# Optimization experiments

Measured on AMD Instinct MI355X. Metric: run time of the kernel, lower is better.

## Reference

```python
import jax, jax.numpy as jnp
import numpy as np

B, QLEN, DIM = 16, 1, 4096
H, HKV, HD = 32, 8, 128  # n_heads, n_kv_heads, head_dim
PREFIX = 8192            # tokens already in the static KV cache


def setup_inputs() -> dict:
    key = jax.random.key(0)
    ks = jax.random.split(key, 7)
    s = 0.02
    return {
        "x": jax.random.normal(ks[0], (B, QLEN, DIM), jnp.float32),
        "cache_k": jax.random.normal(ks[1], (B, PREFIX, HKV, HD), jnp.float32),
        "cache_v": jax.random.normal(ks[2], (B, PREFIX, HKV, HD), jnp.float32),
        "wq": jax.random.normal(ks[3], (H * HD, DIM), jnp.float32) * s,
        "wk": jax.random.normal(ks[4], (HKV * HD, DIM), jnp.float32) * s,
        "wv": jax.random.normal(ks[5], (HKV * HD, DIM), jnp.float32) * s,
        "wo": jax.random.normal(ks[6], (DIM, H * HD), jnp.float32) * s,
    }


def reference(x, cache_k, cache_v, wq, wk, wv, wo):
    """Decode step of AttentionWithKVCache (static cache, GQA).

    Equivalent to: write new K/V at start_pos=PREFIX, attend q over
    cache[:, :PREFIX+QLEN], repeat_kv to expand kv heads, SDPA, out proj.
    """
    b, s, _ = x.shape
    q = (x @ wq.T).reshape(b, s, H, HD)        # [B,S,H,D]
    k_new = (x @ wk.T).reshape(b, s, HKV, HD)  # [B,S,Hkv,D]
    v_new = (x @ wv.T).reshape(b, s, HKV, HD)
    # cache write == concat of prefix with new tokens
    k = jnp.concatenate([cache_k, k_new], axis=1)  # [B,K,Hkv,D]
    v = jnp.concatenate([cache_v, v_new], axis=1)
    rep = H // HKV
    # repeat_kv: expand+reshape repeats each kv head `rep` times consecutively
    k = jnp.repeat(k, rep, axis=2)  # [B,K,H,D]
    v = jnp.repeat(v, rep, axis=2)
    scale = 1.0 / jnp.sqrt(jnp.asarray(HD, dtype=q.dtype))
    scores = jnp.einsum("bqhd,bkhd->bhqk", q, k) * scale
    attn = jax.nn.softmax(scores.astype(jnp.float32), axis=-1).astype(q.dtype)
    out = jnp.einsum("bhqk,bkhd->bqhd", attn, v).reshape(b, s, H * HD)
    return out @ wo.T  # [B,S,DIM]
```

## Files before the change

### kernel.cpp

```cpp
#include <hip/hip_runtime.h>
#include <hip/hip_bf16.h>
#include <cstdint>
#include <cstddef>

#define DIM 4096
#define NB 16
#define NH 32
#define NKV 8
#define HD 128
#define PREFIX 8192
#define CHUNK 1024
#define NCHUNK 8

#define WS_QKV 0
#define WS_ATT (WS_QKV + NB * 6144)
#define WS_ML  (WS_ATT + NB * DIM)
#define WS_OP  (WS_ML + NB * NKV * NCHUNK * 4 * 2)

template <int NW>
__global__ __launch_bounds__(NW * 64) void gemv16(
    const float* __restrict__ W0, const float* __restrict__ W1,
    const float* __restrict__ W2, int b1, int b2,
    const float* __restrict__ X, float* __restrict__ Y,
    int y_stride, int scale_rows, float scale) {
  __shared__ float xs[NB][2048];
  const int tid = threadIdx.x;
  const int wave = tid >> 6, lane = tid & 63;
  const int row_base = blockIdx.x * (NW * 4) + wave * 4;

  const float* Wp;
  if (row_base < b1)       Wp = W0 + (size_t)row_base * DIM;
  else if (row_base < b2)  Wp = W1 + (size_t)(row_base - b1) * DIM;
  else                     Wp = W2 + (size_t)(row_base - b2) * DIM;

  float acc[4][NB];
#pragma unroll
  for (int r = 0; r < 4; ++r)
#pragma unroll
    for (int b = 0; b < NB; ++b) acc[r][b] = 0.0f;

  for (int k0 = 0; k0 < DIM; k0 += 2048) {
    __syncthreads();
#pragma unroll
    for (int i = 0; i < (8192 + NW * 64 - 1) / (NW * 64); ++i) {
      const int idx = tid + i * (NW * 64);
      if (idx < 8192) {
        const int b = idx >> 9, c = idx & 511;
        ((float4*)&xs[b][0])[c] =
            ((const float4*)(X + (size_t)b * DIM + k0))[c];
      }
    }
    __syncthreads();
#pragma unroll 4
    for (int ii = 0; ii < 8; ++ii) {
      const int d = ii * 256 + lane * 4;
      float4 w4[4];
#pragma unroll
      for (int r = 0; r < 4; ++r)
        w4[r] = *(const float4*)(Wp + (size_t)r * DIM + k0 + d);
#pragma unroll
      for (int b = 0; b < NB; ++b) {
        float4 x4 = *(const float4*)&xs[b][d];
#pragma unroll
        for (int r = 0; r < 4; ++r)
          acc[r][b] += w4[r].x * x4.x + w4[r].y * x4.y +
                       w4[r].z * x4.z + w4[r].w * x4.w;
      }
    }
  }

#pragma unroll
  for (int r = 0; r < 4; ++r)
#pragma unroll
    for (int b = 0; b < NB; ++b) {
      float v = acc[r][b];
#pragma unroll
      for (int m = 1; m < 64; m <<= 1) v += __shfl_xor(v, m);
      acc[r][b] = v;
    }
  const int rsel = lane >> 4, bsel = lane & 15;
  float v = 0.0f;
#pragma unroll
  for (int r = 0; r < 4; ++r)
#pragma unroll
    for (int b = 0; b < NB; ++b)
      if (r == rsel && b == bsel) v = acc[r][b];
  const int row = row_base + rsel;
  if (row < scale_rows) v *= scale;
  Y[(size_t)bsel * y_stride + row] = v;
}

__global__ __launch_bounds__(256, 4) void attn_partial(
    const float* __restrict__ K, const float* __restrict__ V,
    const float* __restrict__ qkv, float* __restrict__ opart,
    float* __restrict__ mlpart) {
  __shared__ float sc[4 * CHUNK];
  const int tid = threadIdx.x, wave = tid >> 6, lane = tid & 63;
  const int s = lane & 7, grp = lane >> 3;
  const int bid = blockIdx.x;
  const int chunk = bid & (NCHUNK - 1);
  const int bg = bid >> 3;
  const int g = bg & 7, b = bg >> 3;

  float4 qreg[4][4];
#pragma unroll
  for (int hh = 0; hh < 4; ++hh)
#pragma unroll
    for (int j = 0; j < 4; ++j)
      qreg[hh][j] = *(const float4*)(qkv + (size_t)b * 6144 +
                                     (g * 4 + hh) * HD + j * 32 + s * 4);

  const int kbase = chunk * CHUNK + wave * 256;
  const float* krow0 = K + ((size_t)b * PREFIX * NKV + g) * HD +
                       (size_t)(kbase + grp) * (NKV * HD);

#pragma unroll 2
  for (int it = 0; it < 32; ++it) {
    const float* krow = krow0 + (size_t)it * 8 * (NKV * HD);
    float p0 = 0, p1 = 0, p2 = 0, p3 = 0;
#pragma unroll
    for (int j = 0; j < 4; ++j) {
      float4 k4 = *(const float4*)(krow + j * 32 + s * 4);
      p0 += qreg[0][j].x * k4.x + qreg[0][j].y * k4.y + qreg[0][j].z * k4.z + qreg[0][j].w * k4.w;
      p1 += qreg[1][j].x * k4.x + qreg[1][j].y * k4.y + qreg[1][j].z * k4.z + qreg[1][j].w * k4.w;
      p2 += qreg[2][j].x * k4.x + qreg[2][j].y * k4.y + qreg[2][j].z * k4.z + qreg[2][j].w * k4.w;
      p3 += qreg[3][j].x * k4.x + qreg[3][j].y * k4.y + qreg[3][j].z * k4.z + qreg[3][j].w * k4.w;
    }
#pragma unroll
    for (int mk = 1; mk < 8; mk <<= 1) {
      p0 += __shfl_xor(p0, mk);
      p1 += __shfl_xor(p1, mk);
      p2 += __shfl_xor(p2, mk);
      p3 += __shfl_xor(p3, mk);
    }
    if (s == 0) {
      const int kl = wave * 256 + it * 8 + grp;
      sc[0 * CHUNK + kl] = p0;
      sc[1 * CHUNK + kl] = p1;
      sc[2 * CHUNK + kl] = p2;
      sc[3 * CHUNK + kl] = p3;
    }
  }
  __syncthreads();

  const int h = wave;
  float* sch = &sc[h * CHUNK];
  float4 sv[4];
#pragma unroll
  for (int q = 0; q < 4; ++q) sv[q] = *(const float4*)&sch[q * 256 + lane * 4];
  float m = -1e30f;
#pragma unroll
  for (int q = 0; q < 4; ++q)
    m = fmaxf(m, fmaxf(fmaxf(sv[q].x, sv[q].y), fmaxf(sv[q].z, sv[q].w)));
#pragma unroll
  for (int mk = 1; mk < 64; mk <<= 1) m = fmaxf(m, __shfl_xor(m, mk));
  float lsum = 0.0f;
#pragma unroll
  for (int q = 0; q < 4; ++q) {
    sv[q].x = __expf(sv[q].x - m);
    sv[q].y = __expf(sv[q].y - m);
    sv[q].z = __expf(sv[q].z - m);
    sv[q].w = __expf(sv[q].w - m);
    lsum += sv[q].x + sv[q].y + sv[q].z + sv[q].w;
  }
#pragma unroll
  for (int mk = 1; mk < 64; mk <<= 1) lsum += __shfl_xor(lsum, mk);
#pragma unroll
  for (int q = 0; q < 4; ++q) *(float4*)&sch[q * 256 + lane * 4] = sv[q];

  const int dgrp = lane & 31, kpar = lane >> 5;
  const int d0 = dgrp * 4;
  float4 acc = make_float4(0.f, 0.f, 0.f, 0.f);
  const float* vp = V + ((size_t)b * PREFIX * NKV + g) * HD + d0 +
                    (size_t)(chunk * CHUNK + kpar) * (NKV * HD);
#pragma unroll 8
  for (int kk = 0; kk < CHUNK; kk += 2) {
    const float p = sch[kk + kpar];
    float4 v4 = *(const float4*)(vp + (size_t)kk * (NKV * HD));
    acc.x += p * v4.x; acc.y += p * v4.y;
    acc.z += p * v4.z; acc.w += p * v4.w;
  }
  acc.x += __shfl_xor(acc.x, 32);
  acc.y += __shfl_xor(acc.y, 32);
  acc.z += __shfl_xor(acc.z, 32);
  acc.w += __shfl_xor(acc.w, 32);
  const size_t pidx = (((size_t)(b * NKV + g)) * NCHUNK + chunk) * 4 + h;
  if (lane < 32) *(float4*)(opart + pidx * HD + d0) = acc;
  if (lane == 0) {
    mlpart[pidx * 2 + 0] = m;
    mlpart[pidx * 2 + 1] = lsum;
  }
}

__global__ __launch_bounds__(64) void combine(
    const float* __restrict__ opart, const float* __restrict__ mlpart,
    const float* __restrict__ qkv, float* __restrict__ aout) {
  const int bh = blockIdx.x;
  const int hg = bh & 31, b = bh >> 5;
  const int g = hg >> 2, hh = hg & 3;
  const int lane = threadIdx.x;
  const size_t base = ((size_t)(b * NKV + g)) * NCHUNK;

  const float* qp = qkv + (size_t)b * 6144 + hg * HD;
  const float* kn = qkv + (size_t)b * 6144 + 4096 + g * HD;
  const float* vn = qkv + (size_t)b * 6144 + 5120 + g * HD;
  float2 q2 = *(const float2*)(qp + lane * 2);
  float2 k2 = *(const float2*)(kn + lane * 2);
  float sn = q2.x * k2.x + q2.y * k2.y;
#pragma unroll
  for (int mk = 1; mk < 64; mk <<= 1) sn += __shfl_xor(sn, mk);

  float M = sn;
#pragma unroll
  for (int c = 0; c < NCHUNK; ++c)
    M = fmaxf(M, mlpart[((base + c) * 4 + hh) * 2]);

  float L = 0, ax = 0, ay = 0;
#pragma unroll
  for (int c = 0; c < NCHUNK; ++c) {
    const size_t pidx = (base + c) * 4 + hh;
    const float mc = mlpart[pidx * 2 + 0];
    const float lc = mlpart[pidx * 2 + 1];
    const float w = __expf(mc - M);
    L += lc * w;
    float2 o2 = *(const float2*)(opart + pidx * HD + lane * 2);
    ax += w * o2.x;
    ay += w * o2.y;
  }
  const float pn = __expf(sn - M);
  float2 v2 = *(const float2*)(vn + lane * 2);
  L += pn;
  ax += pn * v2.x;
  ay += pn * v2.y;

  const float inv = 1.0f / L;
  aout[(size_t)b * DIM + hg * HD + lane * 2 + 0] = ax * inv;
  aout[(size_t)b * DIM + hg * HD + lane * 2 + 1] = ay * inv;
}

extern "C" void kernel_launch(void* const* d_in, const int* in_sizes, int n_in,
                              void* d_out, int out_size, void* d_ws,
                              size_t ws_size, hipStream_t stream) {
  const float* x  = (const float*)d_in[0];
  const float* ck = (const float*)d_in[1];
  const float* cv = (const float*)d_in[2];
  const float* wq = (const float*)d_in[3];
  const float* wk = (const float*)d_in[4];
  const float* wv = (const float*)d_in[5];
  const float* wo = (const float*)d_in[6];
  float* out = (float*)d_out;
  float* ws = (float*)d_ws;

  float* qkv = ws + WS_QKV;
  float* att = ws + WS_ATT;
  float* ml  = ws + WS_ML;
  float* op  = ws + WS_OP;

  const float scale = 0.08838834764831845f;

  gemv16<6><<<256, 384, 0, stream>>>(wq, wk, wv, 4096, 5120, x, qkv, 6144,
                                     4096, scale);
  attn_partial<<<NB * NKV * NCHUNK, 256, 0, stream>>>(ck, cv, qkv, op, ml);
  combine<<<NB * NH, 64, 0, stream>>>(op, ml, qkv, att);
  gemv16<4><<<256, 256, 0, stream>>>(wo, wo, wo, 4096, 4096, att, out, 4096,
                                     0, 1.0f);
}
```

Measured before the change: 290.5 us.

## Split attention softmax per wave to read each V row once for all heads

```diff
diff --git a/kernel.cpp b/kernel.cpp
--- a/kernel.cpp
+++ b/kernel.cpp
@@ -11,11 +11,13 @@
 #define PREFIX 8192
 #define CHUNK 1024
 #define NCHUNK 8
+#define WKEYS 256
+#define NPART (NCHUNK * 4)
 
 #define WS_QKV 0
 #define WS_ATT (WS_QKV + NB * 6144)
 #define WS_ML  (WS_ATT + NB * DIM)
-#define WS_OP  (WS_ML + NB * NKV * NCHUNK * 4 * 2)
+#define WS_OP  (WS_ML + NB * NKV * NPART * 4 * 2)
 
 template <int NW>
 __global__ __launch_bounds__(NW * 64) void gemv16(
@@ -94,13 +96,14 @@
     const float* __restrict__ K, const float* __restrict__ V,
     const float* __restrict__ qkv, float* __restrict__ opart,
     float* __restrict__ mlpart) {
-  __shared__ float sc[4 * CHUNK];
+  __shared__ float sc[4][4 * WKEYS];
   const int tid = threadIdx.x, wave = tid >> 6, lane = tid & 63;
   const int s = lane & 7, grp = lane >> 3;
   const int bid = blockIdx.x;
   const int chunk = bid & (NCHUNK - 1);
   const int bg = bid >> 3;
   const int g = bg & 7, b = bg >> 3;
+  float* scw = &sc[wave][0];
 
   float4 qreg[4][4];
 #pragma unroll
@@ -110,7 +113,7 @@
       qreg[hh][j] = *(const float4*)(qkv + (size_t)b * 6144 +
                                      (g * 4 + hh) * HD + j * 32 + s * 4);
 
-  const int kbase = chunk * CHUNK + wave * 256;
+  const int kbase = chunk * CHUNK + wave * WKEYS;
   const float* krow0 = K + ((size_t)b * PREFIX * NKV + g) * HD +
                        (size_t)(kbase + grp) * (NKV * HD);
 
@@ -134,61 +137,76 @@
       p3 += __shfl_xor(p3, mk);
     }
     if (s == 0) {
-      const int kl = wave * 256 + it * 8 + grp;
-      sc[0 * CHUNK + kl] = p0;
-      sc[1 * CHUNK + kl] = p1;
-      sc[2 * CHUNK + kl] = p2;
-      sc[3 * CHUNK + kl] = p3;
-    }
-  }
-  __syncthreads();
-
-  const int h = wave;
-  float* sch = &sc[h * CHUNK];
-  float4 sv[4];
-#pragma unroll
-  for (int q = 0; q < 4; ++q) sv[q] = *(const float4*)&sch[q * 256 + lane * 4];
-  float m = -1e30f;
-#pragma unroll
-  for (int q = 0; q < 4; ++q)
-    m = fmaxf(m, fmaxf(fmaxf(sv[q].x, sv[q].y), fmaxf(sv[q].z, sv[q].w)));
-#pragma unroll
-  for (int mk = 1; mk < 64; mk <<= 1) m = fmaxf(m, __shfl_xor(m, mk));
-  float lsum = 0.0f;
-#pragma unroll
-  for (int q = 0; q < 4; ++q) {
-    sv[q].x = __expf(sv[q].x - m);
-    sv[q].y = __expf(sv[q].y - m);
-    sv[q].z = __expf(sv[q].z - m);
-    sv[q].w = __expf(sv[q].w - m);
-    lsum += sv[q].x + sv[q].y + sv[q].z + sv[q].w;
-  }
-#pragma unroll
-  for (int mk = 1; mk < 64; mk <<= 1) lsum += __shfl_xor(lsum, mk);
-#pragma unroll
-  for (int q = 0; q < 4; ++q) *(float4*)&sch[q * 256 + lane * 4] = sv[q];
+      const int kl = it * 8 + grp;
+      scw[0 * WKEYS + kl] = p0;
+      scw[1 * WKEYS + kl] = p1;
+      scw[2 * WKEYS + kl] = p2;
+      scw[3 * WKEYS + kl] = p3;
+    }
+  }
+  asm volatile("s_waitcnt lgkmcnt(0)" ::: "memory");
+  __builtin_amdgcn_sched_barrier(0);
+
+  float m_h[4], l_h[4];
+#pragma unroll
+  for (int hh = 0; hh < 4; ++hh) {
+    float4 sv = *(const float4*)&scw[hh * WKEYS + lane * 4];
+    float m = fmaxf(fmaxf(sv.x, sv.y), fmaxf(sv.z, sv.w));
+#pragma unroll
+    for (int mk = 1; mk < 64; mk <<= 1) m = fmaxf(m, __shfl_xor(m, mk));
+    float4 pv;
+    pv.x = __expf(sv.x - m);
+    pv.y = __expf(sv.y - m);
+    pv.z = __expf(sv.z - m);
+    pv.w = __expf(sv.w - m);
+    float l = pv.x + pv.y + pv.z + pv.w;
+#pragma unroll
+    for (int mk = 1; mk < 64; mk <<= 1) l += __shfl_xor(l, mk);
+    *(float4*)&scw[hh * WKEYS + lane * 4] = pv;
+    m_h[hh] = m;
+    l_h[hh] = l;
+  }
+  asm volatile("s_waitcnt lgkmcnt(0)" ::: "memory");
+  __builtin_amdgcn_sched_barrier(0);
 
   const int dgrp = lane & 31, kpar = lane >> 5;
   const int d0 = dgrp * 4;
-  float4 acc = make_float4(0.f, 0.f, 0.f, 0.f);
+  float4 acc[4];
+#pragma unroll
+  for (int hh = 0; hh < 4; ++hh) acc[hh] = make_float4(0.f, 0.f, 0.f, 0.f);
   const float* vp = V + ((size_t)b * PREFIX * NKV + g) * HD + d0 +
-                    (size_t)(chunk * CHUNK + kpar) * (NKV * HD);
-#pragma unroll 8
-  for (int kk = 0; kk < CHUNK; kk += 2) {
-    const float p = sch[kk + kpar];
+                    (size_t)(kbase + kpar) * (NKV * HD);
+#pragma unroll 4
+  for (int kk = 0; kk < WKEYS; kk += 2) {
     float4 v4 = *(const float4*)(vp + (size_t)kk * (NKV * HD));
-    acc.x += p * v4.x; acc.y += p * v4.y;
-    acc.z += p * v4.z; acc.w += p * v4.w;
-  }
-  acc.x += __shfl_xor(acc.x, 32);
-  acc.y += __shfl_xor(acc.y, 32);
-  acc.z += __shfl_xor(acc.z, 32);
-  acc.w += __shfl_xor(acc.w, 32);
-  const size_t pidx = (((size_t)(b * NKV + g)) * NCHUNK + chunk) * 4 + h;
-  if (lane < 32) *(float4*)(opart + pidx * HD + d0) = acc;
+#pragma unroll
+    for (int hh = 0; hh < 4; ++hh) {
+      const float p = scw[hh * WKEYS + kk + kpar];
+      acc[hh].x += p * v4.x;
+      acc[hh].y += p * v4.y;
+      acc[hh].z += p * v4.z;
+      acc[hh].w += p * v4.w;
+    }
+  }
+#pragma unroll
+  for (int hh = 0; hh < 4; ++hh) {
+    acc[hh].x += __shfl_xor(acc[hh].x, 32);
+    acc[hh].y += __shfl_xor(acc[hh].y, 32);
+    acc[hh].z += __shfl_xor(acc[hh].z, 32);
+    acc[hh].w += __shfl_xor(acc[hh].w, 32);
+  }
+  const size_t pp = (((size_t)(b * NKV + g)) * NCHUNK + chunk) * 4 + wave;
+  if (lane < 32) {
+#pragma unroll
+    for (int hh = 0; hh < 4; ++hh)
+      *(float4*)(opart + (pp * 4 + hh) * HD + d0) = acc[hh];
+  }
   if (lane == 0) {
-    mlpart[pidx * 2 + 0] = m;
-    mlpart[pidx * 2 + 1] = lsum;
+#pragma unroll
+    for (int hh = 0; hh < 4; ++hh) {
+      mlpart[(pp * 4 + hh) * 2 + 0] = m_h[hh];
+      mlpart[(pp * 4 + hh) * 2 + 1] = l_h[hh];
+    }
   }
 }
 
@@ -199,7 +217,7 @@
   const int hg = bh & 31, b = bh >> 5;
   const int g = hg >> 2, hh = hg & 3;
   const int lane = threadIdx.x;
-  const size_t base = ((size_t)(b * NKV + g)) * NCHUNK;
+  const size_t base = (size_t)(b * NKV + g) * (NPART * 4) + hh;
 
   const float* qp = qkv + (size_t)b * 6144 + hg * HD;
   const float* kn = qkv + (size_t)b * 6144 + 4096 + g * HD;
@@ -211,14 +229,14 @@
   for (int mk = 1; mk < 64; mk <<= 1) sn += __shfl_xor(sn, mk);
 
   float M = sn;
-#pragma unroll
-  for (int c = 0; c < NCHUNK; ++c)
-    M = fmaxf(M, mlpart[((base + c) * 4 + hh) * 2]);
+#pragma unroll 8
+  for (int c = 0; c < NPART; ++c)
+    M = fmaxf(M, mlpart[(base + c * 4) * 2]);
 
   float L = 0, ax = 0, ay = 0;
-#pragma unroll
-  for (int c = 0; c < NCHUNK; ++c) {
-    const size_t pidx = (base + c) * 4 + hh;
+#pragma unroll 8
+  for (int c = 0; c < NPART; ++c) {
+    const size_t pidx = base + c * 4;
     const float mc = mlpart[pidx * 2 + 0];
     const float lc = mlpart[pidx * 2 + 1];
     const float w = __expf(mc - M);
```

Result: faster. 272.7 us (-6.1%).
